# Optimization experiments

Measured on AMD Instinct MI355X. Metric: run time of the kernel, lower is better.

The kernel has to match this reference:

```python
import jax, jax.numpy as jnp
import numpy as np
import math

DIM = 512
HEADS = 8
DIM_HEAD = 64
SCALE = math.sqrt(DIM_HEAD)
EPS = 1e-12


def rms_norm(x, g):
    # F.normalize(x, dim=1) * g * sqrt(dim); x: [B, C, H, W], g: [C]
    inv = jax.lax.rsqrt(jnp.sum(x * x, axis=1, keepdims=True) + EPS)
    return x * inv * g[None, :, None, None] * jnp.asarray(math.sqrt(x.shape[1]), x.dtype)


def setup_inputs() -> dict:
    key = jax.random.key(0)
    k1, k2, k3 = jax.random.split(key, 3)
    B, H, W = 8, 64, 64
    hidden = HEADS * DIM_HEAD
    x = jax.random.normal(k1, (B, DIM, H, W), dtype=jnp.float32)
    w_qkv = jax.random.normal(k2, (3 * hidden, DIM), dtype=jnp.float32) * (1.0 / math.sqrt(DIM))
    w_out = jax.random.normal(k3, (DIM, hidden), dtype=jnp.float32) * (1.0 / math.sqrt(hidden))
    b_out = jnp.zeros((DIM,), dtype=jnp.float32)
    g1 = jnp.ones((DIM,), dtype=jnp.float32)
    g2 = jnp.ones((DIM,), dtype=jnp.float32)
    return {"x": x, "g1": g1, "w_qkv": w_qkv, "w_out": w_out, "b_out": b_out, "g2": g2}


def reference(x, g1, w_qkv, w_out, b_out, g2):
    B, C, H, W = x.shape
    n = H * W
    xn = rms_norm(x, g1)
    # 1x1 conv == channel matmul: [B, 3*hidden, H, W]
    qkv = jnp.einsum('bchw,oc->bohw', xn, w_qkv)
    q, k, v = jnp.split(qkv, 3, axis=1)
    # b (h c) x y -> b h c n
    def to_heads(t):
        return t.reshape(B, HEADS, DIM_HEAD, n)
    q, k, v = to_heads(q), to_heads(k), to_heads(v)
    q = jax.nn.softmax(q, axis=2) / SCALE   # softmax over channel dim d
    k = jax.nn.softmax(k, axis=3)           # softmax over spatial dim n
    context = jnp.einsum('bhdn,bhen->bhde', k, v)   # [B, H, d, e]
    out = jnp.einsum('bhde,bhdn->bhen', context, q) # [B, H, e, n]
    out = out.reshape(B, HEADS * DIM_HEAD, H, W)
    out = jnp.einsum('bchw,oc->bohw', out, w_out) + b_out[None, :, None, None]
    return rms_norm(out, g2)
```

## Files before the change

kernel.cpp:

```cpp
#include <hip/hip_runtime.h>


typedef unsigned short u16;
typedef __attribute__((ext_vector_type(8))) short short8;
typedef __attribute__((ext_vector_type(4))) short short4_t;
typedef __attribute__((ext_vector_type(4))) float f32x4;

static constexpr size_t XN_B = (size_t)512 * 4096;
static constexpr size_t KV_B = (size_t)1024 * 4096;
static constexpr float SQRT512 = 22.62741699796952f;

typedef const __attribute__((address_space(1))) unsigned int gu32;
typedef __attribute__((address_space(3))) unsigned int lu32;

__device__ __forceinline__ float b2f(u16 u){
  union { unsigned u; float f; } x; x.u = ((unsigned)u) << 16; return x.f;
}
__device__ __forceinline__ u16 f2b(float f){
  union { float f; unsigned u; } x; x.f = f;
  unsigned r = x.u + 0x7FFFu + ((x.u >> 16) & 1u);
  return (u16)(r >> 16);
}
__device__ __forceinline__ void gl16(const u16* g, u16* l){
  __builtin_amdgcn_global_load_lds((gu32*)g, (lu32*)l, 16, 0, 0);
}

__global__ __launch_bounds__(256)
void kprep(const float* __restrict__ wqkv, const float* __restrict__ wout,
           const float* __restrict__ g1, u16* __restrict__ dq, u16* __restrict__ dw,
           const float* __restrict__ x, u16* __restrict__ xnT,
           float* __restrict__ sden){
  __shared__ u16 lt[32][514];
  __shared__ float red4[256][4];
  __shared__ float invs[32];
  int bid = blockIdx.x;
  int t = threadIdx.x;
  if (bid < 1024){
    if (bid < 16) sden[bid * 256 + t] = 0.f;
    size_t i = ((size_t)bid * 256 + t) * 4;
    short4_t o;
    if (i < (size_t)786432){
      f32x4 v = *(const f32x4*)(wqkv + i);
      int c = (int)(i & 511);
      #pragma unroll
      for (int j = 0; j < 4; j++) o[j] = (short)f2b(v[j] * g1[c + j] * SQRT512);
      *(short4_t*)(dq + i) = o;
    } else {
      size_t off = i - 786432;
      f32x4 v = *(const f32x4*)(wout + off);
      #pragma unroll
      for (int j = 0; j < 4; j++) o[j] = (short)f2b(v[j]);
      *(short4_t*)(dw + off) = o;
    }
    return;
  }
  int pg0 = (bid - 1024) * 32;
  int b = pg0 >> 12, p0 = pg0 & 4095;
  int pxg = (t & 7) * 4;
  int chunk = t >> 3;
  const float* xp = x + (size_t)b * XN_B + p0 + pxg;
  f32x4 s = {0.f, 0.f, 0.f, 0.f};
  #pragma unroll 4
  for (int c = chunk * 16; c < chunk * 16 + 16; ++c){
    f32x4 v = *(const f32x4*)(xp + (size_t)c * 4096);
    #pragma unroll
    for (int j = 0; j < 4; j++){
      lt[pxg + j][c] = f2b(v[j]);
      s[j] += v[j] * v[j];
    }
  }
  *(f32x4*)red4[t] = s;
  __syncthreads();
  if (t < 32){
    int pg = t >> 2, pe = t & 3;
    float sum = 0.f;
    #pragma unroll
    for (int ch = 0; ch < 32; ch++) sum += red4[ch * 8 + pg][pe];
    invs[t] = rsqrtf(sum + 1e-12f);
  }
  __syncthreads();
  int px2 = t >> 3, c0 = (t & 7) * 8;
  float iv = invs[px2];
  u16* dst = xnT + (size_t)(pg0 + px2) * 512;
  #pragma unroll
  for (int j = 0; j < 8; j++){
    int c = c0 + j * 64;
    short8 o;
    #pragma unroll
    for (int e = 0; e < 8; e++) o[e] = (short)f2b(b2f(lt[px2][c + e]) * iv);
    *(short8*)(dst + c) = o;
  }
}

__global__ __launch_bounds__(256)
void gemm_qkv(const u16* __restrict__ Wkv, const u16* __restrict__ wq,
              const u16* __restrict__ xnT, u16* __restrict__ kvb,
              u16* __restrict__ qT)
{
  constexpr int NT = 8;
  const int bid = blockIdx.x;
  const u16* A; const u16* BT; u16* C;
  int m0, n0; size_t ldc; bool smax;
  if (bid < 2048){
    int ntile = bid & 31, mtile = (bid >> 5) & 7, z = bid >> 8;
    A = Wkv; BT = xnT + (size_t)z * XN_B; C = kvb + (size_t)z * KV_B;
    m0 = mtile * 128; n0 = ntile * 128; ldc = 4096; smax = false;
  } else {
    int idx = bid - 2048;
    int ntile = idx & 3, mtile = idx >> 2;
    A = xnT; BT = wq; C = qT;
    m0 = mtile * 128; n0 = ntile * 128; ldc = 512; smax = true;
  }
  __shared__ u16 As[2][128 * 64];
  __shared__ u16 Bs[2][128 * 64];
  const int tid = threadIdx.x;
  const int srow0 = tid >> 3;
  const int schunk = tid & 7;
  const int lane = tid & 63, wid = tid >> 6;
  const int wr = (wid >> 1) * 64, wc = (wid & 1) * 64;
  const int fr = lane & 15, fq = lane >> 4;
  f32x4 acc[4][4] = {};

  auto STAGE = [&](int s, int t){
    const int k0 = t * 64;
    #pragma unroll
    for (int r = 0; r < 4; r++){
      int row = r * 32 + srow0;
      int gj = (schunk ^ (row & 7)) * 8;
      gl16(A  + (size_t)(m0 + row) * 512 + k0 + gj, &As[s][0] + r * 2048 + tid * 8);
      gl16(BT + (size_t)(n0 + row) * 512 + k0 + gj, &Bs[s][0] + r * 2048 + tid * 8);
    }
  };

  STAGE(0, 0);
  int cur = 0;
  for (int t = 0; t < NT; t++){
    if (t + 1 < NT){
      STAGE(cur ^ 1, t + 1);
      asm volatile("s_waitcnt vmcnt(8)" ::: "memory");
    } else {
      asm volatile("s_waitcnt vmcnt(0)" ::: "memory");
    }
    __builtin_amdgcn_s_barrier();
    __builtin_amdgcn_sched_barrier(0);
    #pragma unroll
    for (int ks = 0; ks < 2; ks++){
      short8 a[4], b[4];
      #pragma unroll
      for (int i = 0; i < 4; i++){
        int ra = wr + i * 16 + fr;
        a[i] = *(const short8*)(&As[cur][0] + ra * 64 + ((ks * 4 + fq) ^ (ra & 7)) * 8);
        int rb = wc + i * 16 + fr;
        b[i] = *(const short8*)(&Bs[cur][0] + rb * 64 + ((ks * 4 + fq) ^ (rb & 7)) * 8);
      }
      #pragma unroll
      for (int i = 0; i < 4; i++)
        #pragma unroll
        for (int j = 0; j < 4; j++)
          acc[i][j] = __builtin_amdgcn_mfma_f32_16x16x32_bf16(a[i], b[j], acc[i][j], 0, 0, 0);
    }
    __builtin_amdgcn_sched_barrier(0);
    __builtin_amdgcn_s_barrier();
    cur ^= 1;
  }

  if (smax){
    #pragma unroll
    for (int i = 0; i < 4; i++)
      #pragma unroll
      for (int e = 0; e < 4; e++){
        float mx = fmaxf(fmaxf(acc[i][0][e], acc[i][1][e]),
                         fmaxf(acc[i][2][e], acc[i][3][e]));
        mx = fmaxf(mx, __shfl_xor(mx, 1));
        mx = fmaxf(mx, __shfl_xor(mx, 2));
        mx = fmaxf(mx, __shfl_xor(mx, 4));
        mx = fmaxf(mx, __shfl_xor(mx, 8));
        float p0 = __expf(acc[i][0][e] - mx);
        float p1 = __expf(acc[i][1][e] - mx);
        float p2 = __expf(acc[i][2][e] - mx);
        float p3 = __expf(acc[i][3][e] - mx);
        float s = p0 + p1 + p2 + p3;
        s += __shfl_xor(s, 1);
        s += __shfl_xor(s, 2);
        s += __shfl_xor(s, 4);
        s += __shfl_xor(s, 8);
        float r = 1.f / (s * 8.0f);
        acc[i][0][e] = p0 * r; acc[i][1][e] = p1 * r;
        acc[i][2][e] = p2 * r; acc[i][3][e] = p3 * r;
      }
  }
  #pragma unroll
  for (int i = 0; i < 4; i++)
    #pragma unroll
    for (int j = 0; j < 4; j++)
      #pragma unroll
      for (int e = 0; e < 4; e++){
        int row = m0 + wr + i * 16 + fq * 4 + e;
        int col = n0 + wc + j * 16 + fr;
        C[(size_t)row * ldc + col] = f2b(acc[i][j][e]);
      }
}

__global__ __launch_bounds__(512)
void gemm_outrms(const u16* __restrict__ qT, const u16* __restrict__ Mb,
                 const float* __restrict__ bias, const float* __restrict__ g2,
                 float* __restrict__ out)
{
  constexpr int NT = 16;
  const int mt = blockIdx.x, z = blockIdx.y;
  const u16* A  = qT + (size_t)z * 4096 * 512;
  const u16* BT = Mb + (size_t)z * 262144;
  const int m0 = mt * 128;

  __shared__ char smem[84480] __attribute__((aligned(16)));
  u16*   As    = (u16*)smem;
  u16*   Bs    = (u16*)(smem + 16384);
  float* trans = (float*)smem;
  float* rsum  = (float*)(smem + 81920);
  float* invr  = (float*)(smem + 83968);

  const int tid = threadIdx.x;
  const int lane = tid & 63, wid = tid >> 6;
  const int wr = (wid >> 2) * 64;
  const int wc = (wid & 3) * 128;
  const int fr = lane & 15, fq = lane >> 4;
  const int srow = tid >> 2, schunk = tid & 3;
  f32x4 acc[4][8] = {};

  auto STAGE = [&](int s, int t){
    const int k0 = t * 32;
    {
      int gj = (schunk ^ ((srow >> 1) & 3)) * 8;
      gl16(A + (size_t)(m0 + srow) * 512 + k0 + gj, As + s * 4096 + tid * 8);
    }
    #pragma unroll
    for (int r = 0; r < 4; r++){
      int row = r * 128 + srow;
      int gj = (schunk ^ ((row >> 1) & 3)) * 8;
      gl16(BT + (size_t)row * 512 + k0 + gj, Bs + s * 16384 + r * 4096 + tid * 8);
    }
  };

  STAGE(0, 0);
  int cur = 0;
  for (int t = 0; t < NT; t++){
    if (t + 1 < NT){
      STAGE(cur ^ 1, t + 1);
      asm volatile("s_waitcnt vmcnt(5)" ::: "memory");
    } else {
      asm volatile("s_waitcnt vmcnt(0)" ::: "memory");
    }
    __builtin_amdgcn_s_barrier();
    __builtin_amdgcn_sched_barrier(0);
    short8 a[4], b[8];
    #pragma unroll
    for (int i = 0; i < 4; i++){
      int ra = wr + i * 16 + fr;
      a[i] = *(const short8*)(As + cur * 4096 + ra * 32 + ((fq ^ ((ra >> 1) & 3)) * 8));
    }
    #pragma unroll
    for (int j = 0; j < 8; j++){
      int rb = wc + j * 16 + fr;
      b[j] = *(const short8*)(Bs + cur * 16384 + rb * 32 + ((fq ^ ((rb >> 1) & 3)) * 8));
    }
    #pragma unroll
    for (int i = 0; i < 4; i++)
      #pragma unroll
      for (int j = 0; j < 8; j++)
        acc[i][j] = __builtin_amdgcn_mfma_f32_16x16x32_bf16(a[i], b[j], acc[i][j], 0, 0, 0);
    __builtin_amdgcn_sched_barrier(0);
    __builtin_amdgcn_s_barrier();
    cur ^= 1;
  }

  float bcol[8], gcol[8];
  #pragma unroll
  for (int j = 0; j < 8; j++){
    int col = wc + j * 16 + fr;
    bcol[j] = bias[col];
    gcol[j] = g2[col] * SQRT512;
  }
  #pragma unroll
  for (int i = 0; i < 4; i++)
    #pragma unroll
    for (int e = 0; e < 4; e++){
      float p = 0.f;
      #pragma unroll
      for (int j = 0; j < 8; j++){
        acc[i][j][e] += bcol[j];
        p += acc[i][j][e] * acc[i][j][e];
      }
      p += __shfl_xor(p, 1); p += __shfl_xor(p, 2);
      p += __shfl_xor(p, 4); p += __shfl_xor(p, 8);
      if (fr == 0) rsum[(wr + i * 16 + fq * 4 + e) * 4 + (wid & 3)] = p;
    }
  __syncthreads();
  if (tid < 128){
    float ss = rsum[tid * 4] + rsum[tid * 4 + 1] + rsum[tid * 4 + 2] + rsum[tid * 4 + 3];
    invr[tid] = rsqrtf(ss + 1e-12f);
  }
  __syncthreads();
  #pragma unroll
  for (int i = 0; i < 4; i++)
    #pragma unroll
    for (int e = 0; e < 4; e++){
      float iv = invr[wr + i * 16 + fq * 4 + e];
      #pragma unroll
      for (int j = 0; j < 8; j++)
        acc[i][j][e] *= iv * gcol[j];
    }
  const int myhalf = wid >> 2;
  const int cbase = tid >> 3, pi = (tid & 7) * 4;
  #pragma unroll
  for (int q = 0; q < 4; q++){
    __syncthreads();
    if (myhalf == (q >> 1)){
      #pragma unroll
      for (int ii = 0; ii < 2; ii++){
        const int i = (q & 1) * 2 + ii;
        const int ro = ii * 16 + fq * 4;
        #pragma unroll
        for (int j = 0; j < 8; j++){
          int col = wc + j * 16 + fr;
          *(f32x4*)&trans[col * 40 + ro] = acc[i][j];
        }
      }
    }
    __syncthreads();
    #pragma unroll
    for (int it = 0; it < 8; it++){
      int cc = it * 64 + cbase;
      f32x4 v = *(const f32x4*)&trans[cc * 40 + pi];
      *(f32x4*)(out + ((size_t)(z * 512 + cc)) * 4096 + m0 + q * 32 + pi) = v;
    }
  }
}

__global__ __launch_bounds__(256)
void gemm_ctx(const u16* __restrict__ kv, float* __restrict__ P,
              float* __restrict__ sden)
{
  constexpr int K = 512;
  const int z = blockIdx.z;
  const int tid = threadIdx.x;
  const int ar = tid >> 2, ac = (tid & 3) * 8;
  int bh = z >> 3, sp = z & 7, b = bh >> 3, h = bh & 7;
  const u16* A  = kv + (size_t)b * KV_B + (size_t)(h * 64) * 4096 + sp * 512;
  const u16* BT = kv + (size_t)b * KV_B + (size_t)(512 + h * 64) * 4096 + sp * 512;
  __shared__ u16 As[64 * 40];
  __shared__ u16 Bs[64 * 40];
  const int wid = tid >> 6, lane = tid & 63;
  const int wr = (wid >> 1) * 32, wc = (wid & 1) * 32;
  const int lr = lane & 15, kb = lane >> 4;
  f32x4 acc[2][2] = {};
  float ssum = 0.f;
  for (int k0 = 0; k0 < K; k0 += 32){
    short8 av = *(const short8*)(A + (size_t)ar * 4096 + k0 + ac);
    short8 ao;
    #pragma unroll
    for (int e = 0; e < 8; e++){
      float ev = __expf(b2f((u16)av[e]));
      ao[e] = (short)f2b(ev);
      ssum += ev;
    }
    *(short8*)(As + ar * 40 + ac) = ao;
    *(short8*)(Bs + ar * 40 + ac) = *(const short8*)(BT + (size_t)ar * 4096 + k0 + ac);
    __syncthreads();
    short8 a0 = *(const short8*)(As + (wr +      lr) * 40 + kb * 8);
    short8 a1 = *(const short8*)(As + (wr + 16 + lr) * 40 + kb * 8);
    short8 b0 = *(const short8*)(Bs + (wc +      lr) * 40 + kb * 8);
    short8 b1 = *(const short8*)(Bs + (wc + 16 + lr) * 40 + kb * 8);
    acc[0][0] = __builtin_amdgcn_mfma_f32_16x16x32_bf16(a0, b0, acc[0][0], 0, 0, 0);
    acc[0][1] = __builtin_amdgcn_mfma_f32_16x16x32_bf16(a0, b1, acc[0][1], 0, 0, 0);
    acc[1][0] = __builtin_amdgcn_mfma_f32_16x16x32_bf16(a1, b0, acc[1][0], 0, 0, 0);
    acc[1][1] = __builtin_amdgcn_mfma_f32_16x16x32_bf16(a1, b1, acc[1][1], 0, 0, 0);
    __syncthreads();
  }
  ssum += __shfl_xor(ssum, 1);
  ssum += __shfl_xor(ssum, 2);
  if ((tid & 3) == 0) atomicAdd(sden + b * 512 + h * 64 + ar, ssum);
  #pragma unroll
  for (int mi = 0; mi < 2; mi++)
    #pragma unroll
    for (int ni = 0; ni < 2; ni++)
      #pragma unroll
      for (int j = 0; j < 4; j++){
        int row = wr + mi * 16 + kb * 4 + j;
        int col = wc + ni * 16 + lr;
        P[(size_t)z * 4096 + (size_t)row * 64 + col] = acc[mi][ni][j];
      }
}

__global__ __launch_bounds__(256)
void kctxw(const float* __restrict__ P, const float* __restrict__ sden,
           const u16* __restrict__ woutbf, u16* __restrict__ M)
{
  const int z = blockIdx.z;
  const int b = z >> 3, h = z & 7;
  const int m0 = blockIdx.y * 64;
  const int tid = threadIdx.x;
  __shared__ u16 As[64 * 72];
  __shared__ u16 Bs[64 * 72];
  {
    int r = tid >> 2, c0 = (tid & 3) * 16;
    const u16* wsrc = woutbf + (size_t)(m0 + r) * 512 + h * 64 + c0;
    *(short8*)(As + r * 72 + c0)     = *(const short8*)(wsrc);
    *(short8*)(As + r * 72 + c0 + 8) = *(const short8*)(wsrc + 8);
    float rs = 1.f / sden[b * 512 + h * 64 + r];
    const float* p = P + (size_t)z * 32768 + (size_t)r * 64 + c0;
    #pragma unroll
    for (int e = 0; e < 16; e++){
      float s = 0.f;
      #pragma unroll
      for (int sp = 0; sp < 8; sp++) s += p[e + sp * 4096];
      Bs[r * 72 + c0 + e] = f2b(s * rs);
    }
  }
  __syncthreads();
  const int wid = tid >> 6, lane = tid & 63;
  const int wr = (wid >> 1) * 32, wc = (wid & 1) * 32;
  const int lr = lane & 15, kb = lane >> 4;
  f32x4 acc[2][2] = {};
  #pragma unroll
  for (int k0 = 0; k0 < 64; k0 += 32){
    short8 a0 = *(const short8*)(As + (wr +      lr) * 72 + k0 + kb * 8);
    short8 a1 = *(const short8*)(As + (wr + 16 + lr) * 72 + k0 + kb * 8);
    short8 b0 = *(const short8*)(Bs + (wc +      lr) * 72 + k0 + kb * 8);
    short8 b1 = *(const short8*)(Bs + (wc + 16 + lr) * 72 + k0 + kb * 8);
    acc[0][0] = __builtin_amdgcn_mfma_f32_16x16x32_bf16(a0, b0, acc[0][0], 0, 0, 0);
    acc[0][1] = __builtin_amdgcn_mfma_f32_16x16x32_bf16(a0, b1, acc[0][1], 0, 0, 0);
    acc[1][0] = __builtin_amdgcn_mfma_f32_16x16x32_bf16(a1, b0, acc[1][0], 0, 0, 0);
    acc[1][1] = __builtin_amdgcn_mfma_f32_16x16x32_bf16(a1, b1, acc[1][1], 0, 0, 0);
  }
  #pragma unroll
  for (int mi = 0; mi < 2; mi++)
    #pragma unroll
    for (int ni = 0; ni < 2; ni++)
      #pragma unroll
      for (int j = 0; j < 4; j++){
        int row = m0 + wr + mi * 16 + kb * 4 + j;
        int col = wc + ni * 16 + lr;
        M[(size_t)b * 262144 + (size_t)row * 512 + h * 64 + col] = f2b(acc[mi][ni][j]);
      }
}

extern "C" void kernel_launch(void* const* d_in, const int* in_sizes, int n_in,
                              void* d_out, int out_size, void* d_ws, size_t ws_size,
                              hipStream_t stream)
{
  (void)in_sizes; (void)n_in; (void)out_size; (void)ws_size;
  const float* x    = (const float*)d_in[0];
  const float* g1   = (const float*)d_in[1];
  const float* wqkv = (const float*)d_in[2];
  const float* wout = (const float*)d_in[3];
  const float* bout = (const float*)d_in[4];
  const float* g2   = (const float*)d_in[5];
  float* out = (float*)d_out;
  char* ws = (char*)d_ws;

  u16*   xnT   = (u16*)(ws);
  float* P     = (float*)(ws);
  u16*   M     = (u16*)(ws + (size_t)8388608);
  u16*   qT    = (u16*)(ws + (size_t)33554432);
  u16*   kv    = (u16*)(ws + (size_t)67108864);
  u16*   wbf   = (u16*)(ws + (size_t)134217728);
  u16*   wkvbf = wbf + (size_t)512 * 512;
  u16*   woutbf= (u16*)(ws + (size_t)135790592);
  float* sden  = (float*)(ws + (size_t)136314880);

  kprep<<<2048, 256, 0, stream>>>(wqkv, wout, g1, wbf, woutbf, x, xnT, sden);
  gemm_qkv<<<3072, 256, 0, stream>>>(wkvbf, wbf, xnT, kv, qT);
  gemm_ctx<<<dim3(1, 1, 512), 256, 0, stream>>>(kv, P, sden);
  kctxw<<<dim3(1, 8, 64), 256, 0, stream>>>(P, sden, woutbf, M);
  gemm_outrms<<<dim3(32, 8), 512, 0, stream>>>(qT, M, bout, g2, out);
}
```

Before: 163.8 us.

## Split fused QKV GEMM into KV kernel with register-loaded weights and 256x256 Q GEMM

The single fused QKV launch is split in two. The K/V GEMM loads the weight operand straight from global memory into registers, cutting its LDS staging in half. The Q projection becomes its own 512-thread kernel with 256x256 tiles, a K-step of 32 and raised MFMA priority, with the channel softmax fused into its epilogue. This aims to cut LDS traffic and improve per-block reuse, at the cost of an extra launch, heavier register pressure, and uncoalesced direct global weight loads.

```diff
diff --git a/kernel.cpp b/kernel.cpp
--- a/kernel.cpp
+++ b/kernel.cpp
@@ -92,26 +92,114 @@
   }
 }
 
+__global__ __launch_bounds__(512)
+void gemm_q(const u16* __restrict__ xnT, const u16* __restrict__ wq,
+            u16* __restrict__ qT)
+{
+  constexpr int NT = 16;
+  const u16* A  = xnT;
+  const u16* BT = wq;
+  const int m0 = blockIdx.y * 256, n0 = blockIdx.x * 256;
+  __shared__ u16 As[2][256 * 32];
+  __shared__ u16 Bs[2][256 * 32];
+  const int tid = threadIdx.x;
+  const int lane = tid & 63, wid = tid >> 6;
+  const int wr = (wid >> 2) * 128, wc = (wid & 3) * 64;
+  const int fr = lane & 15, fq = lane >> 4;
+  const int srow = tid >> 2;
+  const int sslot = tid & 3;
+  f32x4 acc[8][4] = {};
+
+  auto STAGE = [&](int s, int t){
+    const int k0 = t * 32;
+    #pragma unroll
+    for (int r = 0; r < 2; r++){
+      int row = r * 128 + srow;
+      int gj = (sslot ^ ((row >> 1) & 3)) * 8;
+      gl16(A  + (size_t)(m0 + row) * 512 + k0 + gj, &As[s][0] + r * 4096 + tid * 8);
+      gl16(BT + (size_t)(n0 + row) * 512 + k0 + gj, &Bs[s][0] + r * 4096 + tid * 8);
+    }
+  };
+
+  STAGE(0, 0);
+  int cur = 0;
+  for (int t = 0; t < NT; t++){
+    if (t + 1 < NT){
+      STAGE(cur ^ 1, t + 1);
+      asm volatile("s_waitcnt vmcnt(4)" ::: "memory");
+    } else {
+      asm volatile("s_waitcnt vmcnt(0)" ::: "memory");
+    }
+    __builtin_amdgcn_s_barrier();
+    __builtin_amdgcn_sched_barrier(0);
+    short8 a[8], b[4];
+    #pragma unroll
+    for (int i = 0; i < 8; i++){
+      int ra = wr + i * 16 + fr;
+      a[i] = *(const short8*)(&As[cur][0] + ra * 32 + ((fq ^ ((ra >> 1) & 3)) * 8));
+    }
+    #pragma unroll
+    for (int j = 0; j < 4; j++){
+      int rb = wc + j * 16 + fr;
+      b[j] = *(const short8*)(&Bs[cur][0] + rb * 32 + ((fq ^ ((rb >> 1) & 3)) * 8));
+    }
+    __builtin_amdgcn_s_setprio(1);
+    #pragma unroll
+    for (int i = 0; i < 8; i++)
+      #pragma unroll
+      for (int j = 0; j < 4; j++)
+        acc[i][j] = __builtin_amdgcn_mfma_f32_16x16x32_bf16(a[i], b[j], acc[i][j], 0, 0, 0);
+    __builtin_amdgcn_s_setprio(0);
+    __builtin_amdgcn_sched_barrier(0);
+    __builtin_amdgcn_s_barrier();
+    cur ^= 1;
+  }
+
+  #pragma unroll
+  for (int i = 0; i < 8; i++)
+    #pragma unroll
+    for (int e = 0; e < 4; e++){
+      float mx = fmaxf(fmaxf(acc[i][0][e], acc[i][1][e]),
+                       fmaxf(acc[i][2][e], acc[i][3][e]));
+      mx = fmaxf(mx, __shfl_xor(mx, 1));
+      mx = fmaxf(mx, __shfl_xor(mx, 2));
+      mx = fmaxf(mx, __shfl_xor(mx, 4));
+      mx = fmaxf(mx, __shfl_xor(mx, 8));
+      float p0 = __expf(acc[i][0][e] - mx);
+      float p1 = __expf(acc[i][1][e] - mx);
+      float p2 = __expf(acc[i][2][e] - mx);
+      float p3 = __expf(acc[i][3][e] - mx);
+      float s = p0 + p1 + p2 + p3;
+      s += __shfl_xor(s, 1);
+      s += __shfl_xor(s, 2);
+      s += __shfl_xor(s, 4);
+      s += __shfl_xor(s, 8);
+      float r = 1.f / (s * 8.0f);
+      acc[i][0][e] = p0 * r; acc[i][1][e] = p1 * r;
+      acc[i][2][e] = p2 * r; acc[i][3][e] = p3 * r;
+    }
+  #pragma unroll
+  for (int i = 0; i < 8; i++)
+    #pragma unroll
+    for (int j = 0; j < 4; j++)
+      #pragma unroll
+      for (int e = 0; e < 4; e++){
+        int row = m0 + wr + i * 16 + fq * 4 + e;
+        int col = n0 + wc + j * 16 + fr;
+        qT[(size_t)row * 512 + col] = f2b(acc[i][j][e]);
+      }
+}
+
 __global__ __launch_bounds__(256)
-void gemm_qkv(const u16* __restrict__ Wkv, const u16* __restrict__ wq,
-              const u16* __restrict__ xnT, u16* __restrict__ kvb,
-              u16* __restrict__ qT)
+void gemm_kv_ar(const u16* __restrict__ Wkv, const u16* __restrict__ xnT,
+                u16* __restrict__ kvb)
 {
   constexpr int NT = 8;
-  const int bid = blockIdx.x;
-  const u16* A; const u16* BT; u16* C;
-  int m0, n0; size_t ldc; bool smax;
-  if (bid < 2048){
-    int ntile = bid & 31, mtile = (bid >> 5) & 7, z = bid >> 8;
-    A = Wkv; BT = xnT + (size_t)z * XN_B; C = kvb + (size_t)z * KV_B;
-    m0 = mtile * 128; n0 = ntile * 128; ldc = 4096; smax = false;
-  } else {
-    int idx = bid - 2048;
-    int ntile = idx & 3, mtile = idx >> 2;
-    A = xnT; BT = wq; C = qT;
-    m0 = mtile * 128; n0 = ntile * 128; ldc = 512; smax = true;
-  }
-  __shared__ u16 As[2][128 * 64];
+  const int z = blockIdx.z;
+  const u16* A  = Wkv;
+  const u16* BT = xnT + (size_t)z * XN_B;
+  u16* C = kvb + (size_t)z * KV_B;
+  const int m0 = blockIdx.y * 128, n0 = blockIdx.x * 128;
   __shared__ u16 Bs[2][128 * 64];
   const int tid = threadIdx.x;
   const int srow0 = tid >> 3;
@@ -119,25 +207,34 @@
   const int lane = tid & 63, wid = tid >> 6;
   const int wr = (wid >> 1) * 64, wc = (wid & 1) * 64;
   const int fr = lane & 15, fq = lane >> 4;
+  const u16* Arow[4];
+  #pragma unroll
+  for (int i = 0; i < 4; i++)
+    Arow[i] = A + (size_t)(m0 + wr + i * 16 + fr) * 512 + fq * 8;
   f32x4 acc[4][4] = {};
 
-  auto STAGE = [&](int s, int t){
+  auto STAGE_B = [&](int s, int t){
     const int k0 = t * 64;
     #pragma unroll
     for (int r = 0; r < 4; r++){
       int row = r * 32 + srow0;
       int gj = (schunk ^ (row & 7)) * 8;
-      gl16(A  + (size_t)(m0 + row) * 512 + k0 + gj, &As[s][0] + r * 2048 + tid * 8);
       gl16(BT + (size_t)(n0 + row) * 512 + k0 + gj, &Bs[s][0] + r * 2048 + tid * 8);
     }
   };
 
-  STAGE(0, 0);
+  STAGE_B(0, 0);
   int cur = 0;
   for (int t = 0; t < NT; t++){
+    short8 a[2][4];
+    #pragma unroll
+    for (int ks = 0; ks < 2; ks++)
+      #pragma unroll
+      for (int i = 0; i < 4; i++)
+        a[ks][i] = *(const short8*)(Arow[i] + t * 64 + ks * 32);
     if (t + 1 < NT){
-      STAGE(cur ^ 1, t + 1);
-      asm volatile("s_waitcnt vmcnt(8)" ::: "memory");
+      STAGE_B(cur ^ 1, t + 1);
+      asm volatile("s_waitcnt vmcnt(4)" ::: "memory");
     } else {
       asm volatile("s_waitcnt vmcnt(0)" ::: "memory");
     }
@@ -145,11 +242,9 @@
     __builtin_amdgcn_sched_barrier(0);
     #pragma unroll
     for (int ks = 0; ks < 2; ks++){
-      short8 a[4], b[4];
+      short8 b[4];
       #pragma unroll
       for (int i = 0; i < 4; i++){
-        int ra = wr + i * 16 + fr;
-        a[i] = *(const short8*)(&As[cur][0] + ra * 64 + ((ks * 4 + fq) ^ (ra & 7)) * 8);
         int rb = wc + i * 16 + fr;
         b[i] = *(const short8*)(&Bs[cur][0] + rb * 64 + ((ks * 4 + fq) ^ (rb & 7)) * 8);
       }
@@ -157,38 +252,13 @@
       for (int i = 0; i < 4; i++)
         #pragma unroll
         for (int j = 0; j < 4; j++)
-          acc[i][j] = __builtin_amdgcn_mfma_f32_16x16x32_bf16(a[i], b[j], acc[i][j], 0, 0, 0);
+          acc[i][j] = __builtin_amdgcn_mfma_f32_16x16x32_bf16(a[ks][i], b[j], acc[i][j], 0, 0, 0);
     }
     __builtin_amdgcn_sched_barrier(0);
     __builtin_amdgcn_s_barrier();
     cur ^= 1;
   }
 
-  if (smax){
-    #pragma unroll
-    for (int i = 0; i < 4; i++)
-      #pragma unroll
-      for (int e = 0; e < 4; e++){
-        float mx = fmaxf(fmaxf(acc[i][0][e], acc[i][1][e]),
-                         fmaxf(acc[i][2][e], acc[i][3][e]));
-        mx = fmaxf(mx, __shfl_xor(mx, 1));
-        mx = fmaxf(mx, __shfl_xor(mx, 2));
-        mx = fmaxf(mx, __shfl_xor(mx, 4));
-        mx = fmaxf(mx, __shfl_xor(mx, 8));
-        float p0 = __expf(acc[i][0][e] - mx);
-        float p1 = __expf(acc[i][1][e] - mx);
-        float p2 = __expf(acc[i][2][e] - mx);
-        float p3 = __expf(acc[i][3][e] - mx);
-        float s = p0 + p1 + p2 + p3;
-        s += __shfl_xor(s, 1);
-        s += __shfl_xor(s, 2);
-        s += __shfl_xor(s, 4);
-        s += __shfl_xor(s, 8);
-        float r = 1.f / (s * 8.0f);
-        acc[i][0][e] = p0 * r; acc[i][1][e] = p1 * r;
-        acc[i][2][e] = p2 * r; acc[i][3][e] = p3 * r;
-      }
-  }
   #pragma unroll
   for (int i = 0; i < 4; i++)
     #pragma unroll
@@ -197,7 +267,7 @@
       for (int e = 0; e < 4; e++){
         int row = m0 + wr + i * 16 + fq * 4 + e;
         int col = n0 + wc + j * 16 + fr;
-        C[(size_t)row * ldc + col] = f2b(acc[i][j][e]);
+        C[(size_t)row * 4096 + col] = f2b(acc[i][j][e]);
       }
 }
 
@@ -469,7 +539,8 @@
   float* sden  = (float*)(ws + (size_t)136314880);
 
   kprep<<<2048, 256, 0, stream>>>(wqkv, wout, g1, wbf, woutbf, x, xnT, sden);
-  gemm_qkv<<<3072, 256, 0, stream>>>(wkvbf, wbf, xnT, kv, qT);
+  gemm_kv_ar<<<dim3(32, 8, 8), 256, 0, stream>>>(wkvbf, xnT, kv);
+  gemm_q<<<dim3(2, 128, 1), 512, 0, stream>>>(xnT, wbf, qT);
   gemm_ctx<<<dim3(1, 1, 512), 256, 0, stream>>>(kv, P, sden);
   kctxw<<<dim3(1, 8, 64), 256, 0, stream>>>(P, sden, woutbf, M);
   gemm_outrms<<<dim3(32, 8), 512, 0, stream>>>(qT, M, bout, g2, out);
```

New measurement: 200.3 us. +22.3%, slower.
